# Kernel tuning notes

Hardware: AMD Instinct MI355X
Metric: run time of the kernel (lower is better)

Reference implementation:

```python
import jax, jax.numpy as jnp
import numpy as np

B, S, D, H = 8, 512, 1024, 16
HD = D // H                      # head_dim = 64
MAX_SEQ_LEN = 512
SCRATCH_SLOTS = 64


def _rope_cache():
    inv_freq = 1.0 / (10000.0 ** (jnp.arange(0, HD, 2, dtype=jnp.float32) / HD))
    t = jnp.arange(MAX_SEQ_LEN + SCRATCH_SLOTS, dtype=jnp.float32)
    freqs = jnp.outer(t, inv_freq)               # [T, HD//2]
    freqs = jnp.concatenate([freqs, freqs], -1)  # [T, HD]
    return jnp.sin(freqs), jnp.cos(freqs)


def rotate_half(x):
    x1, x2 = x[..., : x.shape[-1] // 2], x[..., x.shape[-1] // 2 :]
    return jnp.concatenate([-x2, x1], axis=-1)


def setup_inputs() -> dict:
    key = jax.random.key(0)
    ks = jax.random.split(key, 5)
    def w(k):
        return jax.random.normal(k, (D, D), dtype=jnp.float32) * 0.02
    return {
        "x": jax.random.normal(ks[0], (B, S, D), dtype=jnp.float32),
        "Wq": w(ks[1]), "bq": jnp.zeros((D,), jnp.float32),
        "Wk": w(ks[2]), "bk": jnp.zeros((D,), jnp.float32),
        "Wv": w(ks[3]), "bv": jnp.zeros((D,), jnp.float32),
        "Wo": w(ks[4]), "bo": jnp.zeros((D,), jnp.float32),
    }


def reference(x, Wq, bq, Wk, bk, Wv, bv, Wo, bo):
    b, s, d = x.shape
    sin_c, cos_c = _rope_cache()
    scale = jnp.array(HD ** (-0.5), dtype=jnp.float32)

    xh = x.astype(jnp.float16)
    def lin(inp, W, bias):  # nnx.Linear with dtype=fp16: cast params + input to fp16
        return inp @ W.astype(jnp.float16) + bias.astype(jnp.float16)

    q = lin(xh, Wq, bq).reshape(b, s, H, HD)
    k = lin(xh, Wk, bk).reshape(b, s, H, HD)
    v = lin(xh, Wv, bv).reshape(b, s, H, HD)

    sin = sin_c[:s, None, :].astype(jnp.float32)  # [s,1,HD]
    cos = cos_c[:s, None, :].astype(jnp.float32)
    qf = q.astype(jnp.float32)
    kf = k.astype(jnp.float32)
    q = qf * cos + rotate_half(qf) * sin
    k = kf * cos + rotate_half(kf) * sin
    v = v.astype(jnp.float32)
    q = q * scale  # module's explicit scale

    # [b,H,s,HD]
    q, k, v = (t.transpose(0, 2, 1, 3) for t in (q, k, v))

    # jax.nn.dot_product_attention additionally scales by 1/sqrt(HD)
    logits = jnp.einsum("bhqd,bhkd->bhqk", q, k) * scale
    probs = jax.nn.softmax(logits, axis=-1)
    out = jnp.einsum("bhqk,bhkd->bhqd", probs, v)
    out = out.transpose(0, 2, 1, 3).reshape(b, s, d)
    return lin(out.astype(jnp.float16), Wo, bo)
```

## Files before the change

### kernel.cpp

```cpp
#include <hip/hip_runtime.h>

typedef _Float16 half8 __attribute__((ext_vector_type(8)));
typedef _Float16 half4v __attribute__((ext_vector_type(4)));
typedef float f32x4 __attribute__((ext_vector_type(4)));

#define OFF_CS    0u
#define OFF_XH    (1u<<20)
#define OFF_WQKVT (OFF_XH + 8u*1024u*1024u)
#define OFF_WOT   (OFF_WQKVT + 8u*1024u*1024u)
#define OFF_QKV   (OFF_WOT + 2u*1024u*1024u)
#define OFF_ATTN  OFF_WQKVT


__device__ __forceinline__ void gload16(const _Float16* g, _Float16* l) {
  __builtin_amdgcn_global_load_lds((const __attribute__((address_space(1))) void*)g,
                                   (__attribute__((address_space(3))) void*)l, 16, 0, 0);
}

__global__ void prep_k(const float* __restrict__ x,
                       const float* __restrict__ W0, const float* __restrict__ W1,
                       const float* __restrict__ W2, const float* __restrict__ W3,
                       _Float16* __restrict__ xh, _Float16* __restrict__ wqkvt,
                       _Float16* __restrict__ wot, float2* __restrict__ cs) {
  int bid = blockIdx.x, tid = threadIdx.x;
  if (bid < 4096) {
    int i = bid * 256 + tid;
    float4 v = ((const float4*)x)[i];
    half4v h;
    h[0] = (_Float16)v.x; h[1] = (_Float16)v.y; h[2] = (_Float16)v.z; h[3] = (_Float16)v.w;
    *(half4v*)(xh + (size_t)i * 4) = h;
  } else if (bid < 8192) {
    __shared__ float tile[32][33];
    int tb = bid - 4096;
    int z = tb >> 10, t = tb & 1023, by = t >> 5, bx = t & 31;
    const float* W = z == 0 ? W0 : z == 1 ? W1 : z == 2 ? W2 : W3;
    _Float16* Wt = z < 3 ? wqkvt + (size_t)z * 1048576 : wot;
    int r = tid >> 3, c0 = (tid & 7) * 4;
    float4 v = *(const float4*)(W + (size_t)(by * 32 + r) * 1024 + bx * 32 + c0);
    tile[r][c0] = v.x; tile[r][c0 + 1] = v.y; tile[r][c0 + 2] = v.z; tile[r][c0 + 3] = v.w;
    __syncthreads();
    half4v h;
#pragma unroll
    for (int j = 0; j < 4; j++) h[j] = (_Float16)tile[c0 + j][r];
    *(half4v*)(Wt + (size_t)(bx * 32 + r) * 1024 + by * 32 + c0) = h;
  } else {
    int idx = (bid - 8192) * 256 + tid;
    int pos = idx >> 5, j = idx & 31;
    float inv = powf(10000.0f, -(float)j * (1.0f / 32.0f));
    float f = (float)pos * inv;
    cs[idx] = make_float2(cosf(f), sinf(f));
  }
}

__global__ __launch_bounds__(512, 1) void gemm384_k(
    const _Float16* __restrict__ A, const _Float16* __restrict__ Bt,
    const float* __restrict__ b0, const float* __restrict__ b1, const float* __restrict__ b2,
    _Float16* __restrict__ C, const float2* __restrict__ cs) {
  __shared__ _Float16 Ar[3][128 * 32];
  __shared__ _Float16 Br[3][384 * 32];

  int bid = blockIdx.x;
  int wgid = (bid & 7) * 32 + (bid >> 3);
  int by = wgid >> 3, bx = wgid & 7;

  int tid = threadIdx.x, lane = tid & 63, w = tid >> 6;
  int wr = w >> 1, wc = w & 1;
  int arow = lane & 15, ag = lane >> 4;
  int s8 = (((arow & 1) << 2) | ag) ^ ((arow >> 1) & 7);

  int qq = (lane & 7) ^ (lane >> 3);
  int rloc = ((lane >> 3) << 1) + (qq >> 2);
  int gcol = (qq & 3) * 8;

  const _Float16* Ag = A + (size_t)(by * 128) * 1024;
  const _Float16* Bg = Bt + (size_t)(bx * 384) * 1024;

  f32x4 acc[2][12] = {};

  auto stage = [&](int t) {
    int slot = t % 3;
    int k0 = t * 32;
    gload16(Ag + (size_t)(w * 16 + rloc) * 1024 + k0 + gcol, &Ar[slot][w * 512]);
#pragma unroll
    for (int i = 0; i < 3; i++) {
      int c = w * 3 + i;
      gload16(Bg + (size_t)(c * 16 + rloc) * 1024 + k0 + gcol, &Br[slot][c * 512]);
    }
  };

  stage(0); stage(1);
  asm volatile("s_waitcnt vmcnt(4)" ::: "memory");
  __builtin_amdgcn_s_barrier();
  __builtin_amdgcn_sched_barrier(0);

  for (int t = 0; t < 32; ++t) {
    if (t < 30) stage(t + 2);
    __builtin_amdgcn_sched_barrier(0);
    const _Float16* Ac = &Ar[t % 3][0];
    const _Float16* Bc = &Br[t % 3][0];
    half8 a[2], b[12];
#pragma unroll
    for (int m = 0; m < 2; m++) {
      int R = wr * 32 + m * 16 + arow;
      a[m] = *(const half8*)&Ac[(R >> 1) * 64 + s8 * 8];
    }
#pragma unroll
    for (int n = 0; n < 12; n++) {
      int R = wc * 192 + n * 16 + arow;
      b[n] = *(const half8*)&Bc[(R >> 1) * 64 + s8 * 8];
    }
    __builtin_amdgcn_s_setprio(1);
#pragma unroll
    for (int m = 0; m < 2; m++)
#pragma unroll
      for (int n = 0; n < 12; n++)
        acc[m][n] = __builtin_amdgcn_mfma_f32_16x16x32_f16(a[m], b[n], acc[m][n], 0, 0, 0);
    __builtin_amdgcn_s_setprio(0);
    __builtin_amdgcn_sched_barrier(0);
    if (t < 30)       asm volatile("s_waitcnt vmcnt(4)" ::: "memory");
    else if (t == 30) asm volatile("s_waitcnt vmcnt(0)" ::: "memory");
    if (t < 31) {
      __builtin_amdgcn_s_barrier();
      __builtin_amdgcn_sched_barrier(0);
    }
  }

  int gc0 = bx * 384 + wc * 192;
#pragma unroll
  for (int g = 0; g < 3; g++) {
    int cb = gc0 + g * 64;
    const float* bp = cb < 1024 ? b0 : (cb < 2048 ? b1 : b2);
    float bb_[4];
#pragma unroll
    for (int n = 0; n < 4; n++) bb_[n] = bp[(cb & 1023) + n * 16 + arow];

    if (cb < 2048) {
      bool isQ = cb < 1024;
#pragma unroll
      for (int m = 0; m < 2; m++) {
        int gr = by * 128 + wr * 32 + m * 16 + ag * 4;
#pragma unroll
        for (int r = 0; r < 4; r++) {
          int row = gr + r, pos = row & 511;
#pragma unroll
          for (int n = 0; n < 2; n++) {
            int j = n * 16 + arow;
            float av = (float)(_Float16)(acc[m][g * 4 + n][r] + bb_[n]);
            float bv = (float)(_Float16)(acc[m][g * 4 + n + 2][r] + bb_[n + 2]);
            float2 tt = cs[pos * 32 + j];
            float o0 = av * tt.x - bv * tt.y;
            float o1 = bv * tt.x + av * tt.y;
            if (isQ) { o0 *= 0.015625f; o1 *= 0.015625f; }
            C[(size_t)row * 3072 + cb + j]      = (_Float16)o0;
            C[(size_t)row * 3072 + cb + j + 32] = (_Float16)o1;
          }
        }
      }
    } else {
#pragma unroll
      for (int m = 0; m < 2; m++) {
        int gr = by * 128 + wr * 32 + m * 16 + ag * 4;
        int bb2 = gr >> 9;
        int st6 = (gr & 511) >> 6;
        int s63 = gr & 63;
#pragma unroll
        for (int n = 0; n < 4; n++) {
          int colh = cb - 2048 + n * 16 + arow;
          int h = colh >> 6, hd = colh & 63;
          half4v v4;
#pragma unroll
          for (int r = 0; r < 4; r++) v4[r] = (_Float16)(acc[m][g * 4 + n][r] + bb_[n]);
          size_t addr = ((size_t)(bb2 * 512 + hd * 8 + st6)) * 3072 + 2048 + h * 64 + s63;
          *(half4v*)(C + addr) = v4;
        }
      }
    }
  }
}

__global__ __launch_bounds__(256, 2) void gemm_out_k(
    const _Float16* __restrict__ A, const _Float16* __restrict__ Bt,
    const float* __restrict__ b0, float* __restrict__ Cv) {
  constexpr int BM = 64;
  __shared__ _Float16 Ar[3][BM * 32];
  __shared__ _Float16 Br[3][128 * 32];

  int nwg = gridDim.x, cpx = nwg >> 3;
  int bid = blockIdx.x;
  int wgid = (bid & 7) * cpx + (bid >> 3);
  int by = wgid / 8, bx = wgid % 8;

  int tid = threadIdx.x, lane = tid & 63, w = tid >> 6;
  int wr = w >> 1, wc = w & 1;
  int arow = lane & 15, ag = lane >> 4;
  int s8 = (((arow & 1) << 2) | ag) ^ ((arow >> 1) & 7);

  int qq = (lane & 7) ^ (lane >> 3);
  int rloc = ((lane >> 3) << 1) + (qq >> 2);
  int gcol = (qq & 3) * 8;

  const _Float16* Ag = A + (size_t)(by * BM) * 1024;
  const _Float16* Bg = Bt + (size_t)(bx * 128) * 1024;

  f32x4 acc[2][4] = {};

  auto stage = [&](int t) {
    int slot = t % 3;
    int k0 = t * 32;
    {
      int c = w;
      if (c < 4)
        gload16(Ag + (size_t)(c * 16 + rloc) * 1024 + k0 + gcol, &Ar[slot][c * 512]);
    }
#pragma unroll
    for (int i = 0; i < 2; i++) {
      int c = w * 2 + i;
      gload16(Bg + (size_t)(c * 16 + rloc) * 1024 + k0 + gcol, &Br[slot][c * 512]);
    }
  };

  stage(0); stage(1);
  asm volatile("s_waitcnt vmcnt(3)" ::: "memory");
  __builtin_amdgcn_s_barrier();
  __builtin_amdgcn_sched_barrier(0);

  for (int t = 0; t < 32; ++t) {
    if (t < 30) stage(t + 2);
    __builtin_amdgcn_sched_barrier(0);
    const _Float16* Ac = &Ar[t % 3][0];
    const _Float16* Bc = &Br[t % 3][0];
    half8 a[2], b[4];
#pragma unroll
    for (int m = 0; m < 2; m++) {
      int R = wr * 32 + m * 16 + arow;
      a[m] = *(const half8*)&Ac[(R >> 1) * 64 + s8 * 8];
    }
#pragma unroll
    for (int n = 0; n < 4; n++) {
      int R = wc * 64 + n * 16 + arow;
      b[n] = *(const half8*)&Bc[(R >> 1) * 64 + s8 * 8];
    }
    __builtin_amdgcn_s_setprio(1);
#pragma unroll
    for (int m = 0; m < 2; m++)
#pragma unroll
      for (int n = 0; n < 4; n++)
        acc[m][n] = __builtin_amdgcn_mfma_f32_16x16x32_f16(a[m], b[n], acc[m][n], 0, 0, 0);
    __builtin_amdgcn_s_setprio(0);
    __builtin_amdgcn_sched_barrier(0);
    if (t < 30)       asm volatile("s_waitcnt vmcnt(3)" ::: "memory");
    else if (t == 30) asm volatile("s_waitcnt vmcnt(0)" ::: "memory");
    if (t < 31) {
      __builtin_amdgcn_s_barrier();
      __builtin_amdgcn_sched_barrier(0);
    }
  }

#pragma unroll
  for (int m = 0; m < 2; m++) {
    int gr = by * BM + wr * 32 + m * 16 + ag * 4;
#pragma unroll
    for (int n = 0; n < 4; n++) {
      int gc = bx * 128 + wc * 64 + n * 16 + arow;
      float bb = b0[gc];
#pragma unroll
      for (int r = 0; r < 4; r++)
        Cv[(size_t)(gr + r) * 1024 + gc] = (float)(_Float16)(acc[m][n][r] + bb);
    }
  }
}

__global__ __launch_bounds__(256, 4) void attn_k(const _Float16* __restrict__ qkv,
                                                 _Float16* __restrict__ out) {
  int id = blockIdx.x;
  int bh = id & 127, qt = id >> 7;
  int b = bh >> 4, h = bh & 15;
  int tid = threadIdx.x, lane = tid & 63, w = tid >> 6;
  int arow = lane & 15, ag = lane >> 4;

  __shared__ _Float16 Ks[64 * 64];
  __shared__ _Float16 Vs[64 * 64];
  __shared__ _Float16 Pl[4][16][72];

  int qrow0 = b * 512 + qt * 64 + w * 16;
  const _Float16* Qp = qkv + (size_t)qrow0 * 3072 + h * 64;
  half8 qa[2];
#pragma unroll
  for (int ks = 0; ks < 2; ks++)
    qa[ks] = *(const half8*)(Qp + (size_t)arow * 3072 + ks * 32 + ag * 8);

  const _Float16* Kb = qkv + (size_t)(b * 512) * 3072 + 1024 + h * 64;

  int srow = lane >> 3;
  int sslot = (lane & 7) ^ srow;
  const _Float16* Ksrc0 = Kb + (size_t)(w * 16 + srow) * 3072 + sslot * 8;
  const _Float16* Vsrc0 = qkv + ((size_t)(b * 512) + (w * 16 + srow) * 8) * 3072
                          + 2048 + h * 64 + sslot * 8;

  int rs = arow & 7;

  float psl[4] = {0.f, 0.f, 0.f, 0.f};
  f32x4 oacc[4] = {};

  for (int st = 0; st < 8; ++st) {
#pragma unroll
    for (int i = 0; i < 2; i++) {
      gload16(Ksrc0 + (size_t)(st * 64 + i * 8) * 3072, &Ks[(w * 16 + i * 8) * 64]);
      gload16(Vsrc0 + (size_t)(i * 64 + st) * 3072,     &Vs[(w * 16 + i * 8) * 64]);
    }
    __syncthreads();

    f32x4 lg[4];
#pragma unroll
    for (int c = 0; c < 4; c++) {
      f32x4 a0 = {};
#pragma unroll
      for (int ks = 0; ks < 2; ks++) {
        int slot = (ks * 4 + ag) ^ rs;
        half8 kb = *(const half8*)&Ks[(c * 16 + arow) * 64 + slot * 8];
        a0 = __builtin_amdgcn_mfma_f32_16x16x32_f16(qa[ks], kb, a0, 0, 0, 0);
      }
      lg[c] = a0;
    }
    _Float16 ph[4][4];
#pragma unroll
    for (int r = 0; r < 4; r++) {
#pragma unroll
      for (int c = 0; c < 4; c++) {
        float p = __builtin_amdgcn_exp2f(lg[c][r] * 1.44269504f);
        psl[r] += p;
        ph[c][r] = (_Float16)p;
      }
    }
#pragma unroll
    for (int c = 0; c < 4; c++)
#pragma unroll
      for (int r = 0; r < 4; r++) Pl[w][ag * 4 + r][c * 16 + arow] = ph[c][r];
#pragma unroll
    for (int ks = 0; ks < 2; ks++) {
      half8 pa = *(const half8*)&Pl[w][arow][ks * 32 + ag * 8];
#pragma unroll
      for (int c = 0; c < 4; c++) {
        int slot = (ks * 4 + ag) ^ rs;
        half8 vb = *(const half8*)&Vs[(c * 16 + arow) * 64 + slot * 8];
        oacc[c] = __builtin_amdgcn_mfma_f32_16x16x32_f16(pa, vb, oacc[c], 0, 0, 0);
      }
    }
    __syncthreads();
  }
#pragma unroll
  for (int r = 0; r < 4; r++)
#pragma unroll
    for (int d = 1; d < 16; d <<= 1) psl[r] += __shfl_xor(psl[r], d, 16);
#pragma unroll
  for (int c = 0; c < 4; c++)
#pragma unroll
    for (int r = 0; r < 4; r++) {
      float v = oacc[c][r] / psl[r];
      out[(size_t)(qrow0 + ag * 4 + r) * 1024 + h * 64 + c * 16 + arow] = (_Float16)v;
    }
}

extern "C" void kernel_launch(void* const* d_in, const int* in_sizes, int n_in,
                              void* d_out, int out_size, void* d_ws, size_t ws_size,
                              hipStream_t stream) {
  const float* x  = (const float*)d_in[0];
  const float* Wq = (const float*)d_in[1];
  const float* bq = (const float*)d_in[2];
  const float* Wk = (const float*)d_in[3];
  const float* bk = (const float*)d_in[4];
  const float* Wv = (const float*)d_in[5];
  const float* bv = (const float*)d_in[6];
  const float* Wo = (const float*)d_in[7];
  const float* bo = (const float*)d_in[8];

  char* ws = (char*)d_ws;
  float2* cs      = (float2*)(ws + OFF_CS);
  _Float16* xh    = (_Float16*)(ws + OFF_XH);
  _Float16* wqkvt = (_Float16*)(ws + OFF_WQKVT);
  _Float16* wot   = (_Float16*)(ws + OFF_WOT);
  _Float16* qkv   = (_Float16*)(ws + OFF_QKV);
  _Float16* attn  = (_Float16*)(ws + OFF_ATTN);

  prep_k<<<8256, 256, 0, stream>>>(x, Wq, Wk, Wv, Wo, xh, wqkvt, wot, cs);
  gemm384_k<<<256, 512, 0, stream>>>(xh, wqkvt, bq, bk, bv, qkv, cs);
  attn_k<<<1024, 256, 0, stream>>>(qkv, attn);
  gemm_out_k<<<512, 256, 0, stream>>>(attn, wot, bo, (float*)d_out);
}
```

Baseline: 98.55 us.

## Retile QKV GEMM into 128x64 tiles with more, smaller workgroups

The QKV projection GEMM changes from 256 workgroups of 512 threads, each computing a 128x384 tile, to 1536 workgroups of 256 threads, each computing a 128x64 tile. Launch bounds now allow four workgroups per CU, and the load split and waitcnt counts are adjusted to match. The goal is higher occupancy and better latency hiding across CUs. In exchange, the A operand is reloaded far more often, so per-tile data reuse drops and global/L2 traffic rises.

```diff
diff --git a/kernel.cpp b/kernel.cpp
--- a/kernel.cpp
+++ b/kernel.cpp
@@ -52,19 +52,18 @@
   }
 }
 
-__global__ __launch_bounds__(512, 1) void gemm384_k(
+__global__ __launch_bounds__(256, 4) void gemm_qkv_k(
     const _Float16* __restrict__ A, const _Float16* __restrict__ Bt,
     const float* __restrict__ b0, const float* __restrict__ b1, const float* __restrict__ b2,
     _Float16* __restrict__ C, const float2* __restrict__ cs) {
   __shared__ _Float16 Ar[3][128 * 32];
-  __shared__ _Float16 Br[3][384 * 32];
+  __shared__ _Float16 Br[3][64 * 32];
 
   int bid = blockIdx.x;
-  int wgid = (bid & 7) * 32 + (bid >> 3);
-  int by = wgid >> 3, bx = wgid & 7;
+  int wgid = (bid & 7) * 192 + (bid >> 3);
+  int by = wgid / 48, bx = wgid % 48;
 
   int tid = threadIdx.x, lane = tid & 63, w = tid >> 6;
-  int wr = w >> 1, wc = w & 1;
   int arow = lane & 15, ag = lane >> 4;
   int s8 = (((arow & 1) << 2) | ag) ^ ((arow >> 1) & 7);
 
@@ -73,23 +72,23 @@
   int gcol = (qq & 3) * 8;
 
   const _Float16* Ag = A + (size_t)(by * 128) * 1024;
-  const _Float16* Bg = Bt + (size_t)(bx * 384) * 1024;
-
-  f32x4 acc[2][12] = {};
+  const _Float16* Bg = Bt + (size_t)(bx * 64) * 1024;
+
+  f32x4 acc[2][4] = {};
 
   auto stage = [&](int t) {
     int slot = t % 3;
     int k0 = t * 32;
-    gload16(Ag + (size_t)(w * 16 + rloc) * 1024 + k0 + gcol, &Ar[slot][w * 512]);
-#pragma unroll
-    for (int i = 0; i < 3; i++) {
-      int c = w * 3 + i;
-      gload16(Bg + (size_t)(c * 16 + rloc) * 1024 + k0 + gcol, &Br[slot][c * 512]);
-    }
+#pragma unroll
+    for (int i = 0; i < 2; i++) {
+      int c = w * 2 + i;
+      gload16(Ag + (size_t)(c * 16 + rloc) * 1024 + k0 + gcol, &Ar[slot][c * 512]);
+    }
+    gload16(Bg + (size_t)(w * 16 + rloc) * 1024 + k0 + gcol, &Br[slot][w * 512]);
   };
 
   stage(0); stage(1);
-  asm volatile("s_waitcnt vmcnt(4)" ::: "memory");
+  asm volatile("s_waitcnt vmcnt(3)" ::: "memory");
   __builtin_amdgcn_s_barrier();
   __builtin_amdgcn_sched_barrier(0);
 
@@ -98,26 +97,26 @@
     __builtin_amdgcn_sched_barrier(0);
     const _Float16* Ac = &Ar[t % 3][0];
     const _Float16* Bc = &Br[t % 3][0];
-    half8 a[2], b[12];
+    half8 a[2], b[4];
 #pragma unroll
     for (int m = 0; m < 2; m++) {
-      int R = wr * 32 + m * 16 + arow;
+      int R = w * 32 + m * 16 + arow;
       a[m] = *(const half8*)&Ac[(R >> 1) * 64 + s8 * 8];
     }
 #pragma unroll
-    for (int n = 0; n < 12; n++) {
-      int R = wc * 192 + n * 16 + arow;
+    for (int n = 0; n < 4; n++) {
+      int R = n * 16 + arow;
       b[n] = *(const half8*)&Bc[(R >> 1) * 64 + s8 * 8];
     }
     __builtin_amdgcn_s_setprio(1);
 #pragma unroll
     for (int m = 0; m < 2; m++)
 #pragma unroll
-      for (int n = 0; n < 12; n++)
+      for (int n = 0; n < 4; n++)
         acc[m][n] = __builtin_amdgcn_mfma_f32_16x16x32_f16(a[m], b[n], acc[m][n], 0, 0, 0);
     __builtin_amdgcn_s_setprio(0);
     __builtin_amdgcn_sched_barrier(0);
-    if (t < 30)       asm volatile("s_waitcnt vmcnt(4)" ::: "memory");
+    if (t < 30)       asm volatile("s_waitcnt vmcnt(3)" ::: "memory");
     else if (t == 30) asm volatile("s_waitcnt vmcnt(0)" ::: "memory");
     if (t < 31) {
       __builtin_amdgcn_s_barrier();
@@ -125,54 +124,50 @@
     }
   }
 
-  int gc0 = bx * 384 + wc * 192;
-#pragma unroll
-  for (int g = 0; g < 3; g++) {
-    int cb = gc0 + g * 64;
-    const float* bp = cb < 1024 ? b0 : (cb < 2048 ? b1 : b2);
-    float bb_[4];
-#pragma unroll
-    for (int n = 0; n < 4; n++) bb_[n] = bp[(cb & 1023) + n * 16 + arow];
-
-    if (cb < 2048) {
-      bool isQ = cb < 1024;
-#pragma unroll
-      for (int m = 0; m < 2; m++) {
-        int gr = by * 128 + wr * 32 + m * 16 + ag * 4;
-#pragma unroll
-        for (int r = 0; r < 4; r++) {
-          int row = gr + r, pos = row & 511;
-#pragma unroll
-          for (int n = 0; n < 2; n++) {
-            int j = n * 16 + arow;
-            float av = (float)(_Float16)(acc[m][g * 4 + n][r] + bb_[n]);
-            float bv = (float)(_Float16)(acc[m][g * 4 + n + 2][r] + bb_[n + 2]);
-            float2 tt = cs[pos * 32 + j];
-            float o0 = av * tt.x - bv * tt.y;
-            float o1 = bv * tt.x + av * tt.y;
-            if (isQ) { o0 *= 0.015625f; o1 *= 0.015625f; }
-            C[(size_t)row * 3072 + cb + j]      = (_Float16)o0;
-            C[(size_t)row * 3072 + cb + j + 32] = (_Float16)o1;
-          }
+  int gc0 = bx * 64;
+  const float* bp = gc0 < 1024 ? b0 : (gc0 < 2048 ? b1 : b2);
+  float bb_[4];
+#pragma unroll
+  for (int n = 0; n < 4; n++) bb_[n] = bp[(gc0 & 1023) + n * 16 + arow];
+
+  if (gc0 < 2048) {
+    bool isQ = gc0 < 1024;
+#pragma unroll
+    for (int m = 0; m < 2; m++) {
+      int gr = by * 128 + w * 32 + m * 16 + ag * 4;
+#pragma unroll
+      for (int r = 0; r < 4; r++) {
+        int row = gr + r, pos = row & 511;
+#pragma unroll
+        for (int n = 0; n < 2; n++) {
+          int j = n * 16 + arow;
+          float av = (float)(_Float16)(acc[m][n][r] + bb_[n]);
+          float bv = (float)(_Float16)(acc[m][n + 2][r] + bb_[n + 2]);
+          float2 tt = cs[pos * 32 + j];
+          float o0 = av * tt.x - bv * tt.y;
+          float o1 = bv * tt.x + av * tt.y;
+          if (isQ) { o0 *= 0.015625f; o1 *= 0.015625f; }
+          C[(size_t)row * 3072 + gc0 + j]      = (_Float16)o0;
+          C[(size_t)row * 3072 + gc0 + j + 32] = (_Float16)o1;
         }
       }
-    } else {
-#pragma unroll
-      for (int m = 0; m < 2; m++) {
-        int gr = by * 128 + wr * 32 + m * 16 + ag * 4;
-        int bb2 = gr >> 9;
-        int st6 = (gr & 511) >> 6;
-        int s63 = gr & 63;
-#pragma unroll
-        for (int n = 0; n < 4; n++) {
-          int colh = cb - 2048 + n * 16 + arow;
-          int h = colh >> 6, hd = colh & 63;
-          half4v v4;
-#pragma unroll
-          for (int r = 0; r < 4; r++) v4[r] = (_Float16)(acc[m][g * 4 + n][r] + bb_[n]);
-          size_t addr = ((size_t)(bb2 * 512 + hd * 8 + st6)) * 3072 + 2048 + h * 64 + s63;
-          *(half4v*)(C + addr) = v4;
-        }
+    }
+  } else {
+#pragma unroll
+    for (int m = 0; m < 2; m++) {
+      int gr = by * 128 + w * 32 + m * 16 + ag * 4;
+      int bb2 = gr >> 9;
+      int st6 = (gr & 511) >> 6;
+      int s63 = gr & 63;
+#pragma unroll
+      for (int n = 0; n < 4; n++) {
+        int colh = gc0 - 2048 + n * 16 + arow;
+        int h = colh >> 6, hd = colh & 63;
+        half4v v4;
+#pragma unroll
+        for (int r = 0; r < 4; r++) v4[r] = (_Float16)(acc[m][n][r] + bb_[n]);
+        size_t addr = ((size_t)(bb2 * 512 + hd * 8 + st6)) * 3072 + 2048 + h * 64 + s63;
+        *(half4v*)(C + addr) = v4;
       }
     }
   }
@@ -207,11 +202,8 @@
   auto stage = [&](int t) {
     int slot = t % 3;
     int k0 = t * 32;
-    {
-      int c = w;
-      if (c < 4)
-        gload16(Ag + (size_t)(c * 16 + rloc) * 1024 + k0 + gcol, &Ar[slot][c * 512]);
-    }
+    if (w < 4)
+      gload16(Ag + (size_t)(w * 16 + rloc) * 1024 + k0 + gcol, &Ar[slot][w * 512]);
 #pragma unroll
     for (int i = 0; i < 2; i++) {
       int c = w * 2 + i;
@@ -383,7 +375,7 @@
   _Float16* attn  = (_Float16*)(ws + OFF_ATTN);
 
   prep_k<<<8256, 256, 0, stream>>>(x, Wq, Wk, Wv, Wo, xh, wqkvt, wot, cs);
-  gemm384_k<<<256, 512, 0, stream>>>(xh, wqkvt, bq, bk, bv, qkv, cs);
+  gemm_qkv_k<<<1536, 256, 0, stream>>>(xh, wqkvt, bq, bk, bv, qkv, cs);
   attn_k<<<1024, 256, 0, stream>>>(qkv, attn);
   gemm_out_k<<<512, 256, 0, stream>>>(attn, wot, bo, (float*)d_out);
 }
```

Measured after the change: 104.0 us. 1.06x slower.
